# Optimization experiments

Hardware: AMD Instinct MI355X
Metric: run time of the kernel (lower is better)

## Reference

```python
import jax, jax.numpy as jnp
import numpy as np

N_USER = 150_000
M_ITEM = 30_000
N_NODES = N_USER + M_ITEM
D = 64                      # embedding_dim
N_LAYERS = 3                # gcn_layer_number
E = 600_000                 # user-item interactions (symmetric nnz = 2E)
B = 1024
NUM_RATE, NUM_GENRE, NUM_DIR, NUM_ACT = 6, 25, 2186, 8030
NUM_GENDER, NUM_AGE, NUM_OCC, NUM_ZIP = 2, 7, 21, 3402
H1, H2 = 64, 64             # first/second fc hidden dims
FC1_IN = D * 10


def setup_inputs() -> dict:
    key = jax.random.key(0)
    ks = jax.random.split(key, 24)
    # aux features: 0/1 values are valid indices for every categorical field
    aux_info = jax.random.randint(ks[0], (B, 10246), 0, 2, dtype=jnp.int32)
    user_ids = jax.random.randint(ks[1], (B,), 0, N_USER, dtype=jnp.int32)
    item_ids = jax.random.randint(ks[2], (B,), 0, M_ITEM, dtype=jnp.int32)
    # bipartite graph: random interactions, symmetric normalized adjacency
    u = jax.random.randint(ks[3], (E,), 0, N_USER, dtype=jnp.int32)
    i = jax.random.randint(ks[4], (E,), 0, M_ITEM, dtype=jnp.int32) + N_USER
    graph_row = jnp.concatenate([u, i])
    graph_col = jnpph = jnp.concatenate([i, u]) if False else jnp.concatenate([i, u])
    deg = jax.ops.segment_sum(jnp.ones((2 * E,), jnp.float32), graph_row, num_segments=N_NODES)
    dinv = jnp.where(deg > 0, jax.lax.rsqrt(jnp.maximum(deg, 1.0)), 0.0)
    graph_val = dinv[graph_row] * dinv[graph_col]
    s = 0.1
    nrm = lambda k, shp: (jax.random.normal(k, shp, jnp.float32) * s)
    return {
        "aux_info": aux_info, "user_ids": user_ids, "item_ids": item_ids,
        "graph_row": graph_row, "graph_col": graph_col, "graph_val": graph_val,
        "rate_tab": nrm(ks[5], (NUM_RATE, D)),
        "genre_W": nrm(ks[6], (NUM_GENRE, D)),
        "director_W": nrm(ks[7], (NUM_DIR, D)),
        "actor_W": nrm(ks[8], (NUM_ACT, D)),
        "gender_tab": nrm(ks[9], (NUM_GENDER, D)),
        "age_tab": nrm(ks[10], (NUM_AGE, D)),
        "occ_tab": nrm(ks[11], (NUM_OCC, D)),
        "area_tab": nrm(ks[12], (NUM_ZIP, D)),
        "user_rel": nrm(ks[13], (N_USER, D)),
        "item_rel": nrm(ks[14], (M_ITEM, D)),
        "fc1_W": nrm(ks[15], (FC1_IN, H1)), "fc1_b": jnp.zeros((H1,), jnp.float32),
        "fc2_W": nrm(ks[16], (H1, H2)), "fc2_b": jnp.zeros((H2,), jnp.float32),
        "out_W": nrm(ks[17], (H2, 1)), "out_b": jnp.zeros((1,), jnp.float32),
    }


def _lightgcn(user_rel, item_rel, row, col, val):
    # LightGCN: repeated SpMM D^-1/2 A D^-1/2 @ emb, mean over layer outputs
    emb = jnp.concatenate([user_rel, item_rel], axis=0)      # [N, D]
    acc = emb
    for _ in range(N_LAYERS):
        emb = jax.ops.segment_sum(val[:, None] * emb[col], row, num_segments=N_NODES)
        acc = acc + emb
    light = acc / (N_LAYERS + 1)
    return light[:N_USER], light[N_USER:]


def _multi_hot(idx_int, W):
    x = idx_int.astype(jnp.float32)
    return (x @ W) / jnp.sum(x, axis=1, keepdims=True)


def reference(aux_info, user_ids, item_ids, graph_row, graph_col, graph_val,
              rate_tab, genre_W, director_W, actor_W,
              gender_tab, age_tab, occ_tab, area_tab,
              user_rel, item_rel,
              fc1_W, fc1_b, fc2_W, fc2_b, out_W, out_b):
    rate_idx = aux_info[:, 0]
    genre_idx = aux_info[:, 1:26]
    director_idx = aux_info[:, 26:2212]
    actor_idx = aux_info[:, 2212:10242]
    gender_idx = aux_info[:, 10242]
    age_idx = aux_info[:, 10243]
    occ_idx = aux_info[:, 10244]
    area_idx = aux_info[:, 10245]

    item_emb = jnp.concatenate([
        rate_tab[rate_idx],
        _multi_hot(genre_idx, genre_W),
        _multi_hot(director_idx, director_W),
        _multi_hot(actor_idx, actor_W),
    ], axis=1)                                               # [B, 4D]
    user_emb = jnp.concatenate([
        gender_tab[gender_idx], age_tab[age_idx],
        occ_tab[occ_idx], area_tab[area_idx],
    ], axis=1)                                               # [B, 4D]

    all_users, all_items = _lightgcn(user_rel, item_rel, graph_row, graph_col, graph_val)
    X = jnp.concatenate([item_emb, user_emb,
                         all_users[user_ids], all_items[item_ids]], axis=1)  # [B, 10D]
    X = jax.nn.relu(X @ fc1_W + fc1_b)
    X = jax.nn.relu(X @ fc2_W + fc2_b)
    return X @ out_W + out_b                                 # [B, 1]
```

## Files before the change

### kernel.cpp

```cpp
#include <hip/hip_runtime.h>
#include <hip/hip_bf16.h>
#include <hip/hip_fp16.h>

#define N_USER 150000
#define M_ITEM 30000
#define N_NODES 180000
#define E2 1200000
#define BATCH 1024
#define AUX_W 10246
#define KP_G 32
#define KP_D 2208
#define KP_A 8064
#define NBKT 265
#define WT_BLKS 2576
#define BCNT_BLKS 293
#define MH_BLKS 672
#define CVT_BLKS 5625

typedef __attribute__((ext_vector_type(8))) short short8;
typedef __attribute__((ext_vector_type(8))) unsigned short ushort8_t;
typedef __attribute__((ext_vector_type(4))) float f32x4;

__device__ __forceinline__ int bucket_of(int r) {
    return r < N_USER ? (r >> 10) : 147 + ((r - N_USER) >> 8);
}

__device__ __forceinline__ int detect_f32(const void* probe) {
    float v = __bfloat162float(((const __hip_bfloat16*)probe)[threadIdx.x & 63]);
    unsigned long long m = __ballot(!(fabsf(v) < 1000.0f));
    return __popcll(m) > 8;
}

struct CvtSeg { const void* src; float* dst; int n; int blk0; };
struct CvtBatch { CvtSeg seg[16]; };

__global__ void __launch_bounds__(256) k_prep(CvtBatch cb, int cvtBlks,
                                              const void* Wg, const void* Wd, const void* Wa,
                                              unsigned short* WtG, unsigned short* WtD, unsigned short* WtA,
                                              const int* __restrict__ grow, int* __restrict__ bucket_tot,
                                              const void* probe) {
    int blk = blockIdx.x, tid = threadIdx.x;
    if (blk < BCNT_BLKS) {
        __shared__ int h[NBKT];
        for (int i = tid; i < NBKT; i += 256) h[i] = 0;
        __syncthreads();
        int idx0 = blk * 4096;
        #pragma unroll
        for (int k = 0; k < 16; ++k) {
            int i = idx0 + k * 256 + tid;
            if (i < E2) atomicAdd(&h[bucket_of(grow[i])], 1);
        }
        __syncthreads();
        for (int i = tid; i < NBKT; i += 256) if (h[i]) atomicAdd(&bucket_tot[i], h[i]);
        return;
    }
    if (blk < BCNT_BLKS + cvtBlks) {
        int isf32 = detect_f32(probe);
        int cblk = blk - BCNT_BLKS;
        int si = 0;
        #pragma unroll
        for (int i = 0; i < 16; ++i) if (cblk >= cb.seg[i].blk0) si = i;
        const CvtSeg sg = cb.seg[si];
        int i = (cblk - sg.blk0) * 256 + tid;
        if (i >= sg.n) return;
        if (isf32) sg.dst[i] = ((const float*)sg.src)[i];
        else       sg.dst[i] = __bfloat162float(((const __hip_bfloat16*)sg.src)[i]);
        return;
    }
    {
        int isf32 = detect_f32(probe);
        int t = (blk - BCNT_BLKS - cvtBlks) * 256 + tid;
        if (t >= (KP_G + KP_D + KP_A) * 64) return;
        int kp = t >> 6, n = t & 63;
        int k, K; const void* src; unsigned short* dst;
        if (kp < KP_G)              { k = kp;               K = 25;   src = Wg; dst = WtG; }
        else if (kp < KP_G + KP_D)  { k = kp - KP_G;        K = 2186; src = Wd; dst = WtD; }
        else                        { k = kp - KP_G - KP_D; K = 8030; src = Wa; dst = WtA; }
        unsigned short v = 0;
        if (k < K) {
            if (isf32) {
                __hip_bfloat16 h = __float2bfloat16(((const float*)src)[(size_t)k * 64 + n]);
                v = *(unsigned short*)&h;
            } else {
                v = ((const unsigned short*)src)[(size_t)k * 64 + n];
            }
        }
        dst[(((size_t)(k >> 5) * 64 + n) * 4 + ((k >> 3) & 3)) * 8 + (k & 7)] = v;
    }
}

__global__ void __launch_bounds__(512) k_bscan(const int* __restrict__ bucket_tot,
                                               int* __restrict__ bucket_base,
                                               int* __restrict__ bucketcur) {
    __shared__ int s[512];
    int tid = threadIdx.x;
    s[tid] = (tid < NBKT) ? bucket_tot[tid] : 0;
    __syncthreads();
    for (int off = 1; off < 512; off <<= 1) {
        int v = (tid >= off) ? s[tid - off] : 0;
        __syncthreads();
        s[tid] += v;
        __syncthreads();
    }
    int excl = tid ? s[tid - 1] : 0;
    bucket_base[tid] = excl;
    if (tid < NBKT) bucketcur[tid] = excl;
}

__device__ void mhgemm_body(int blk, const int* __restrict__ aux,
                            const unsigned short* __restrict__ WtG,
                            const unsigned short* __restrict__ WtD,
                            const unsigned short* __restrict__ WtA,
                            float* __restrict__ Xmh, float* __restrict__ cntf) {
    int seg, rb, k0, klen, Kseg, auxoff;
    const unsigned short* Wt;
    if (blk < 16)       { seg = 0; rb = blk;                      k0 = 0;              klen = 25;                  Kseg = 25;   auxoff = 1;    Wt = WtG; }
    else if (blk < 160) { int t = blk - 16;  seg = 1; rb = t & 15; k0 = (t >> 4) * 256; klen = min(256, 2186 - k0); Kseg = 2186; auxoff = 26;   Wt = WtD; }
    else                { int t = blk - 160; seg = 2; rb = t & 15; k0 = (t >> 4) * 256; klen = min(256, 8030 - k0); Kseg = 8030; auxoff = 2212; Wt = WtA; }
    int lane = threadIdx.x & 63, wave = threadIdx.x >> 6;
    int m = lane & 15, quad = lane >> 4;
    int row = rb * 64 + wave * 16 + m;
    const int* arow = aux + (size_t)row * AUX_W + auxoff;

    f32x4 acc0 = {0.f,0.f,0.f,0.f}, acc1 = acc0, acc2 = acc0, acc3 = acc0;
    int isum = 0;
    int nchunk = (klen + 31) >> 5;
    int pa[8], na[8];
    auto lda = [&](int kci, int (&A)[8]) {
        int kb = k0 + kci * 32 + quad * 8;
        if (kb + 8 <= Kseg) {
            #pragma unroll
            for (int j = 0; j < 8; ++j) A[j] = arow[kb + j];
        } else {
            #pragma unroll
            for (int j = 0; j < 8; ++j) A[j] = (kb + j < Kseg) ? arow[kb + j] : 0;
        }
    };
    lda(0, pa);
    for (int kci = 0; kci < nchunk; ++kci) {
        if (kci + 1 < nchunk) lda(kci + 1, na);
        union { unsigned u[4]; short8 s; } af;
        af.u[0] = (unsigned)pa[0] * 16256u + (unsigned)pa[1] * 0x3F800000u;
        af.u[1] = (unsigned)pa[2] * 16256u + (unsigned)pa[3] * 0x3F800000u;
        af.u[2] = (unsigned)pa[4] * 16256u + (unsigned)pa[5] * 0x3F800000u;
        af.u[3] = (unsigned)pa[6] * 16256u + (unsigned)pa[7] * 0x3F800000u;
        isum += pa[0] + pa[1] + pa[2] + pa[3] + pa[4] + pa[5] + pa[6] + pa[7];
        size_t kcg = (size_t)(k0 >> 5) + kci;
        const unsigned short* bp = Wt + ((kcg * 64 + m) * 4 + quad) * 8;
        short8 b0 = *(const short8*)(bp);
        short8 b1 = *(const short8*)(bp + 512);
        short8 b2 = *(const short8*)(bp + 1024);
        short8 b3 = *(const short8*)(bp + 1536);
        acc0 = __builtin_amdgcn_mfma_f32_16x16x32_bf16(af.s, b0, acc0, 0, 0, 0);
        acc1 = __builtin_amdgcn_mfma_f32_16x16x32_bf16(af.s, b1, acc1, 0, 0, 0);
        acc2 = __builtin_amdgcn_mfma_f32_16x16x32_bf16(af.s, b2, acc2, 0, 0, 0);
        acc3 = __builtin_amdgcn_mfma_f32_16x16x32_bf16(af.s, b3, acc3, 0, 0, 0);
        #pragma unroll
        for (int j = 0; j < 8; ++j) pa[j] = na[j];
    }
    float asum = (float)isum;
    asum += __shfl_xor(asum, 16);
    asum += __shfl_xor(asum, 32);
    if (quad == 0) atomicAdd(&cntf[seg * BATCH + row], asum);
    float* xbase = Xmh + ((size_t)seg * BATCH + rb * 64 + wave * 16 + quad * 4) * 64;
    #pragma unroll
    for (int reg = 0; reg < 4; ++reg) {
        float* xr = xbase + (size_t)reg * 64;
        atomicAdd(&xr[ 0 + m], acc0[reg]);
        atomicAdd(&xr[16 + m], acc1[reg]);
        atomicAdd(&xr[32 + m], acc2[reg]);
        atomicAdd(&xr[48 + m], acc3[reg]);
    }
}

__global__ void __launch_bounds__(256) k_p1(const int* __restrict__ grow, const int* __restrict__ gcol,
                                            int* __restrict__ bucketcur, int2* __restrict__ binned,
                                            const int* __restrict__ aux,
                                            const unsigned short* __restrict__ WtG,
                                            const unsigned short* __restrict__ WtD,
                                            const unsigned short* __restrict__ WtA,
                                            float* __restrict__ Xmh, float* __restrict__ cntf,
                                            const void* rawU, const void* rawI,
                                            __half* __restrict__ embH) {
    int blk = blockIdx.x;
    if (blk < MH_BLKS) {
        mhgemm_body(blk, aux, WtG, WtD, WtA, Xmh, cntf);
        return;
    }
    if (blk < MH_BLKS + BCNT_BLKS) {
        __shared__ int h1[NBKT], base1[NBKT];
        int tid = threadIdx.x;
        for (int i = tid; i < NBKT; i += 256) h1[i] = 0;
        __syncthreads();
        int idx0 = (blk - MH_BLKS) * 4096;
        int r[16], c[16];
        #pragma unroll
        for (int k = 0; k < 16; ++k) {
            int i = idx0 + k * 256 + tid;
            if (i < E2) {
                r[k] = grow[i]; c[k] = gcol[i];
                atomicAdd(&h1[bucket_of(r[k])], 1);
            } else r[k] = -1;
        }
        __syncthreads();
        for (int i = tid; i < NBKT; i += 256) {
            base1[i] = h1[i] ? atomicAdd(&bucketcur[i], h1[i]) : 0;
            h1[i] = 0;
        }
        __syncthreads();
        #pragma unroll
        for (int k = 0; k < 16; ++k) {
            if (r[k] >= 0) {
                int b = bucket_of(r[k]);
                int p = base1[b] + atomicAdd(&h1[b], 1);
                binned[p] = make_int2(r[k], c[k]);
            }
        }
        return;
    }
    int isf32 = detect_f32(rawU);
    int q = (blk - MH_BLKS - BCNT_BLKS) * 256 + threadIdx.x;
    if (q >= N_NODES * 8) return;
    int r = q >> 3;
    const void* src; size_t qq;
    if (r < N_USER) { src = rawU; qq = (size_t)q; }
    else            { src = rawI; qq = (size_t)q - (size_t)N_USER * 8; }
    float f[8];
    if (isf32) {
        float4 a = ((const float4*)src)[qq * 2], b = ((const float4*)src)[qq * 2 + 1];
        f[0]=a.x; f[1]=a.y; f[2]=a.z; f[3]=a.w; f[4]=b.x; f[5]=b.y; f[6]=b.z; f[7]=b.w;
    } else {
        ushort8_t u = ((const ushort8_t*)src)[qq];
        #pragma unroll
        for (int i = 0; i < 8; ++i) {
            unsigned short us = u[i];
            f[i] = __bfloat162float(*(__hip_bfloat16*)&us);
        }
    }
    ushort8_t o;
    #pragma unroll
    for (int i = 0; i < 8; ++i) {
        __half h = __float2half(f[i]);
        o[i] = *(unsigned short*)&h;
    }
    ((ushort8_t*)embH)[(size_t)q] = o;
}

__global__ void __launch_bounds__(256) k_p2(const int2* __restrict__ binned, const int* __restrict__ bb,
                                            int* __restrict__ cols, int2* __restrict__ moffs,
                                            float* __restrict__ dinv, float* __restrict__ dsq,
                                            float* __restrict__ gsc) {
    __shared__ int h[1024];
    __shared__ int ws2[256];
    int b = blockIdx.x, tid = threadIdx.x;
    int r0, r1;
    if (b < 147) { r0 = b << 10; r1 = min((b + 1) << 10, N_USER); }
    else         { r0 = N_USER + ((b - 147) << 8); r1 = min(N_USER + ((b - 146) << 8), N_NODES); }
    int s0 = bb[b], e0 = bb[b + 1];
    for (int i = tid; i < 1024; i += 256) h[i] = 0;
    __syncthreads();
    for (int j = s0 + tid; j < e0; j += 256) atomicAdd(&h[binned[j].x - r0], 1);
    __syncthreads();
    int t0 = tid * 4;
    int a0 = h[t0], a1 = h[t0 + 1], a2 = h[t0 + 2], a3 = h[t0 + 3];
    ws2[tid] = a0 + a1 + a2 + a3;
    __syncthreads();
    for (int off = 1; off < 256; off <<= 1) {
        int v = (tid >= off) ? ws2[tid - off] : 0;
        __syncthreads();
        ws2[tid] += v;
        __syncthreads();
    }
    int excl = tid ? ws2[tid - 1] : 0;
    int ex[4] = { excl, excl + a0, excl + a0 + a1, excl + a0 + a1 + a2 };
    int ac[4] = { a0, a1, a2, a3 };
    #pragma unroll
    for (int i = 0; i < 4; ++i) {
        int row = r0 + t0 + i;
        if (row < r1) {
            moffs[row] = make_int2(s0 + ex[i], s0 + ex[i] + ac[i]);
            float deg = (float)ac[i];
            bool nz = deg > 0.f;
            dinv[row] = nz ? rsqrtf(deg) : 0.f;
            dsq[row]  = nz ? 1.f / deg  : 0.f;
            gsc[row]  = nz ? sqrtf(deg) : 0.f;
        }
        h[t0 + i] = ex[i];
    }
    __syncthreads();
    for (int j = s0 + tid; j < e0; j += 256) {
        int2 e = binned[j];
        int p = s0 + atomicAdd(&h[e.x - r0], 1);
        cols[p] = e.y << 7;
    }
}

__global__ void __launch_bounds__(256, 8) k_spmv_w(const __half* __restrict__ src,
                                                   const void* rawU, const void* rawI,
                                                   __half* __restrict__ dst,
                                                   const int2* __restrict__ moffs_in,
                                                   const int* __restrict__ cols,
                                                   const float* __restrict__ dinv,
                                                   const float* __restrict__ dsq,
                                                   int spmvN, float* __restrict__ tacc,
                                                   const int* __restrict__ uids, const int* __restrict__ iids,
                                                   int2* __restrict__ moffs2) {
    int tid = threadIdx.x, lane = tid & 63;
    int blk = blockIdx.x;
    if (blk >= spmvN) {
        if (blk < spmvN + 512) {
            int t = (blk - spmvN) * 4 + (tid >> 6);
            int r = (t < BATCH) ? uids[t] : (N_USER + iids[t - BATCH]);
            int2 se = moffs_in[r];
            if (lane == 0) moffs2[r] = se;
            for (int j = se.x + lane; j < se.y; j += 64) {
                int c = (unsigned)cols[j] >> 7;
                moffs2[c] = moffs_in[c];
            }
            return;
        }
        {
            int isf32 = detect_f32(rawU);
            int t = (blk - spmvN - 512) * 4 + (tid >> 6);
            const void* s; size_t ri;
            if (t < BATCH) { s = rawU; ri = (size_t)uids[t]; }
            else           { s = rawI; ri = (size_t)iids[t - BATCH]; }
            float v;
            if (isf32) v = ((const float*)s)[ri * 64 + lane];
            else       v = __bfloat162float(((const __hip_bfloat16*)s)[ri * 64 + lane]);
            tacc[(size_t)t * 64 + lane] = v;
            return;
        }
    }
    int wid8 = blk * 4 + (tid >> 6);
    int g = lane >> 3, l8 = lane & 7;
    int r = wid8 * 8 + g;
    int2 se = moffs_in[r];
    int s = se.x, e = se.y;
    const char* sb = (const char*)src + (l8 << 4);
    float a[8] = {0.f,0.f,0.f,0.f,0.f,0.f,0.f,0.f};
    int j0 = s;
    for (; j0 + 4 <= e; j0 += 4) {
        int c[4]; float w[4];
        #pragma unroll
        for (int u = 0; u < 4; ++u) { c[u] = cols[j0 + u]; w[u] = dinv[(unsigned)c[u] >> 7]; }
        float4 rv[4];
        #pragma unroll
        for (int u = 0; u < 4; ++u) rv[u] = *(const float4*)(sb + (size_t)(unsigned)c[u]);
        #pragma unroll
        for (int u = 0; u < 4; ++u) {
            const __half2* h = (const __half2*)&rv[u];
            float2 f0 = __half22float2(h[0]), f1 = __half22float2(h[1]);
            float2 f2 = __half22float2(h[2]), f3 = __half22float2(h[3]);
            a[0] = fmaf(w[u], f0.x, a[0]); a[1] = fmaf(w[u], f0.y, a[1]);
            a[2] = fmaf(w[u], f1.x, a[2]); a[3] = fmaf(w[u], f1.y, a[3]);
            a[4] = fmaf(w[u], f2.x, a[4]); a[5] = fmaf(w[u], f2.y, a[5]);
            a[6] = fmaf(w[u], f3.x, a[6]); a[7] = fmaf(w[u], f3.y, a[7]);
        }
    }
    if (j0 < e) {
        int c[4]; float w[4];
        #pragma unroll
        for (int u = 0; u < 4; ++u) {
            int j = j0 + u;
            c[u] = cols[min(j, e - 1)];
            w[u] = (j < e) ? dinv[(unsigned)c[u] >> 7] : 0.f;
        }
        float4 rv[4];
        #pragma unroll
        for (int u = 0; u < 4; ++u) rv[u] = *(const float4*)(sb + (size_t)(unsigned)c[u]);
        #pragma unroll
        for (int u = 0; u < 4; ++u) {
            const __half2* h = (const __half2*)&rv[u];
            float2 f0 = __half22float2(h[0]), f1 = __half22float2(h[1]);
            float2 f2 = __half22float2(h[2]), f3 = __half22float2(h[3]);
            a[0] = fmaf(w[u], f0.x, a[0]); a[1] = fmaf(w[u], f0.y, a[1]);
            a[2] = fmaf(w[u], f1.x, a[2]); a[3] = fmaf(w[u], f1.y, a[3]);
            a[4] = fmaf(w[u], f2.x, a[4]); a[5] = fmaf(w[u], f2.y, a[5]);
            a[6] = fmaf(w[u], f3.x, a[6]); a[7] = fmaf(w[u], f3.y, a[7]);
        }
    }
    if (e > s) {
        float d = dsq[r];
        float4 ov;
        __half2* op = (__half2*)&ov;
        op[0] = __floats2half2_rn(a[0] * d, a[1] * d);
        op[1] = __floats2half2_rn(a[2] * d, a[3] * d);
        op[2] = __floats2half2_rn(a[4] * d, a[5] * d);
        op[3] = __floats2half2_rn(a[6] * d, a[7] * d);
        *(float4*)((char*)dst + ((size_t)r << 7) + (l8 << 4)) = ov;
    }
}

__global__ void __launch_bounds__(256, 8) k_spmv(const __half* __restrict__ src, __half* __restrict__ dst,
                                                 const int2* __restrict__ moffs_in, const int* __restrict__ cols,
                                                 const float* __restrict__ dsq,
                                                 int spmvN, float* __restrict__ tacc,
                                                 const int* __restrict__ uids, const int* __restrict__ iids,
                                                 const float* __restrict__ gsc) {
    int tid = threadIdx.x, lane = tid & 63;
    int blk = blockIdx.x;
    if (blk >= spmvN) {
        int t = (blk - spmvN) * 4 + (tid >> 6);
        int r = (t < BATCH) ? uids[t] : (N_USER + iids[t - BATCH]);
        float g = gsc[r];
        float h = __half2float(src[(size_t)r * 64 + lane]);
        tacc[(size_t)t * 64 + lane] += (g > 0.f) ? h * g : 0.f;
        return;
    }
    int wid8 = blk * 4 + (tid >> 6);
    int g = lane >> 3, l8 = lane & 7;
    int r = wid8 * 8 + g;
    int2 se = moffs_in[r];
    int s = se.x, e = se.y;
    const char* sb = (const char*)src + (l8 << 4);
    float2 a0 = {0.f,0.f}, a1 = a0, a2 = a0, a3 = a0;
    int j0 = s;
    for (; j0 + 4 <= e; j0 += 4) {
        int c[4];
        #pragma unroll
        for (int u = 0; u < 4; ++u) c[u] = cols[j0 + u];
        float4 rv[4];
        #pragma unroll
        for (int u = 0; u < 4; ++u) rv[u] = *(const float4*)(sb + (size_t)(unsigned)c[u]);
        #pragma unroll
        for (int u = 0; u < 4; ++u) {
            const __half2* h = (const __half2*)&rv[u];
            float2 f0 = __half22float2(h[0]), f1 = __half22float2(h[1]);
            float2 f2 = __half22float2(h[2]), f3 = __half22float2(h[3]);
            a0.x += f0.x; a0.y += f0.y; a1.x += f1.x; a1.y += f1.y;
            a2.x += f2.x; a2.y += f2.y; a3.x += f3.x; a3.y += f3.y;
        }
    }
    if (j0 < e) {
        int c[4]; float w[4];
        #pragma unroll
        for (int u = 0; u < 4; ++u) {
            int j = j0 + u;
            c[u] = cols[min(j, e - 1)];
            w[u] = (j < e) ? 1.f : 0.f;
        }
        float4 rv[4];
        #pragma unroll
        for (int u = 0; u < 4; ++u) rv[u] = *(const float4*)(sb + (size_t)(unsigned)c[u]);
        #pragma unroll
        for (int u = 0; u < 4; ++u) {
            const __half2* h = (const __half2*)&rv[u];
            float2 f0 = __half22float2(h[0]), f1 = __half22float2(h[1]);
            float2 f2 = __half22float2(h[2]), f3 = __half22float2(h[3]);
            a0.x = fmaf(w[u], f0.x, a0.x); a0.y = fmaf(w[u], f0.y, a0.y);
            a1.x = fmaf(w[u], f1.x, a1.x); a1.y = fmaf(w[u], f1.y, a1.y);
            a2.x = fmaf(w[u], f2.x, a2.x); a2.y = fmaf(w[u], f2.y, a2.y);
            a3.x = fmaf(w[u], f3.x, a3.x); a3.y = fmaf(w[u], f3.y, a3.y);
        }
    }
    if (e > s) {
        float d = dsq[r];
        float4 ov;
        __half2* op = (__half2*)&ov;
        op[0] = __floats2half2_rn(a0.x * d, a0.y * d);
        op[1] = __floats2half2_rn(a1.x * d, a1.y * d);
        op[2] = __floats2half2_rn(a2.x * d, a2.y * d);
        op[3] = __floats2half2_rn(a3.x * d, a3.y * d);
        *(float4*)((char*)dst + ((size_t)r << 7) + (l8 << 4)) = ov;
    }
}

__global__ void __launch_bounds__(256) k_mlp(const int* __restrict__ aux,
                                             const float* __restrict__ ratef, const float* __restrict__ genderf,
                                             const float* __restrict__ agef, const float* __restrict__ occf,
                                             const float* __restrict__ areaf, const float* __restrict__ tacc,
                                             const float* __restrict__ Xmh, const float* __restrict__ cntf,
                                             const float* __restrict__ W1, const float* __restrict__ b1,
                                             const float* __restrict__ W2, const float* __restrict__ b2,
                                             const float* __restrict__ Wo, const float* __restrict__ bo,
                                             void* __restrict__ out, const void* probe,
                                             const __half* __restrict__ embA,
                                             const int2* __restrict__ moffs, const int* __restrict__ cols,
                                             const float* __restrict__ dinv, const float* __restrict__ gsc,
                                             const int* __restrict__ uids, const int* __restrict__ iids) {
    __shared__ float sx[4][640];
    __shared__ float sh[4][64];
    int isf32 = detect_f32(probe);
    int lane = threadIdx.x & 63, w = threadIdx.x >> 6;
    int b = blockIdx.x * 4 + w;
    const int* arow = aux + (size_t)b * AUX_W;
    float* xr = sx[w];

    #pragma unroll 1
    for (int which = 0; which < 2; ++which) {
        int t = which ? (BATCH + b) : b;
        int r = which ? (N_USER + iids[b]) : uids[b];
        int2 se = moffs[r];
        int s = se.x, e = se.y;
        int p = lane & 31, ep = lane >> 5;
        const char* sb = (const char*)embA + (p << 2);
        float ax = 0.f, ay = 0.f;
        int j0 = s;
        for (; j0 + 16 <= e; j0 += 16) {
            int c[8];
            #pragma unroll
            for (int u = 0; u < 8; ++u) c[u] = cols[j0 + 2 * u + ep];
            float2 v[8];
            #pragma unroll
            for (int u = 0; u < 8; ++u) v[u] = __half22float2(*(const __half2*)(sb + (size_t)(unsigned)c[u]));
            #pragma unroll
            for (int u = 0; u < 8; ++u) { ax += v[u].x; ay += v[u].y; }
        }
        if (j0 + 8 <= e) {
            int c[4];
            #pragma unroll
            for (int u = 0; u < 4; ++u) c[u] = cols[j0 + 2 * u + ep];
            float2 v[4];
            #pragma unroll
            for (int u = 0; u < 4; ++u) v[u] = __half22float2(*(const __half2*)(sb + (size_t)(unsigned)c[u]));
            #pragma unroll
            for (int u = 0; u < 4; ++u) { ax += v[u].x; ay += v[u].y; }
            j0 += 8;
        }
        if (j0 + 4 <= e) {
            int c0 = cols[j0 + ep], c1 = cols[j0 + 2 + ep];
            float2 v0 = __half22float2(*(const __half2*)(sb + (size_t)(unsigned)c0));
            float2 v1 = __half22float2(*(const __half2*)(sb + (size_t)(unsigned)c1));
            ax += v0.x + v1.x; ay += v0.y + v1.y;
            j0 += 4;
        }
        if (j0 < e) {
            int j1 = j0 + ep, j2 = j0 + 2 + ep;
            int c0 = cols[min(j1, e - 1)], c1 = cols[min(j2, e - 1)];
            float w0 = (j1 < e) ? 1.f : 0.f, w1 = (j2 < e) ? 1.f : 0.f;
            float2 v0 = __half22float2(*(const __half2*)(sb + (size_t)(unsigned)c0));
            float2 v1 = __half22float2(*(const __half2*)(sb + (size_t)(unsigned)c1));
            ax = fmaf(w0, v0.x, ax); ay = fmaf(w0, v0.y, ay);
            ax = fmaf(w1, v1.x, ax); ay = fmaf(w1, v1.y, ay);
        }
        ax += __shfl_xor(ax, 32);
        ay += __shfl_xor(ay, 32);
        if (ep == 0) {
            float s0 = tacc[(size_t)t * 64 + (p << 1)];
            float s1 = tacc[(size_t)t * 64 + (p << 1) + 1];
            if (e > s) {
                float2 self = __half22float2(*(const __half2*)((const char*)embA + ((size_t)r << 7) + (p << 2)));
                float di = dinv[r], g = gsc[r];
                s0 += di * ax + g * self.x;
                s1 += di * ay + g * self.y;
            }
            xr[512 + (which << 6) + (p << 1)]     = s0 * 0.25f;
            xr[512 + (which << 6) + (p << 1) + 1] = s1 * 0.25f;
        }
    }

    xr[0   + lane] = ratef[arow[0] * 64 + lane];
    xr[64  + lane] = Xmh[((size_t)0 * BATCH + b) * 64 + lane] / cntf[0 * BATCH + b];
    xr[128 + lane] = Xmh[((size_t)1 * BATCH + b) * 64 + lane] / cntf[1 * BATCH + b];
    xr[192 + lane] = Xmh[((size_t)2 * BATCH + b) * 64 + lane] / cntf[2 * BATCH + b];
    xr[256 + lane] = genderf[arow[10242] * 64 + lane];
    xr[320 + lane] = agef[arow[10243] * 64 + lane];
    xr[384 + lane] = occf[arow[10244] * 64 + lane];
    xr[448 + lane] = areaf[arow[10245] * 64 + lane];
    float acc = b1[lane];
    #pragma unroll 8
    for (int k = 0; k < 640; ++k) acc += xr[k] * W1[(size_t)k * 64 + lane];
    float h1 = fmaxf(acc, 0.f);
    sh[w][lane] = h1;
    float acc2 = b2[lane];
    #pragma unroll 8
    for (int j = 0; j < 64; ++j) acc2 += sh[w][j] * W2[(size_t)j * 64 + lane];
    float h2 = fmaxf(acc2, 0.f);
    float p = h2 * Wo[lane];
    #pragma unroll
    for (int off = 32; off; off >>= 1) p += __shfl_down(p, off);
    if (lane == 0) {
        float r = p + bo[0];
        if (isf32) ((float*)out)[b] = r;
        else       ((__hip_bfloat16*)out)[b] = __float2bfloat16(r);
    }
}

extern "C" void kernel_launch(void* const* d_in, const int* in_sizes, int n_in,
                              void* d_out, int out_size, void* d_ws, size_t ws_size,
                              hipStream_t stream) {
    const int* aux  = (const int*)d_in[0];
    const int* uids = (const int*)d_in[1];
    const int* iids = (const int*)d_in[2];
    const int* grow = (const int*)d_in[3];
    const int* gcol = (const int*)d_in[4];

    char* p = (char*)d_ws;
    auto alloc = [&](size_t bytes) -> char* {
        char* r = p;
        p += (bytes + 255) / 256 * 256;
        return r;
    };
    int*   bucket_tot  = (int*)alloc(512 * 4);
    float* Xmh         = (float*)alloc((size_t)3 * BATCH * 64 * 4);
    float* cntf        = (float*)alloc((size_t)3 * BATCH * 4);
    int2*  moffs2      = (int2*)alloc((size_t)180224 * 8);
    char*  zero_end    = p;
    int*   bucket_base = (int*)alloc(512 * 4);
    int*   bucketcur   = (int*)alloc(512 * 4);
    int2*  moffs       = (int2*)alloc((size_t)180224 * 8);
    float* dinv        = (float*)alloc((size_t)180224 * 4);
    float* dsq         = (float*)alloc((size_t)180224 * 4);
    float* gsc         = (float*)alloc((size_t)180224 * 4);
    int2*  binned      = (int2*)alloc((size_t)E2 * 8);
    int*   cols        = (int*)alloc((size_t)E2 * 4);
    __half* embH       = (__half*)alloc((size_t)N_NODES * 64 * 2);
    __half* embA       = (__half*)alloc((size_t)N_NODES * 64 * 2);
    __half* embB       = (__half*)alloc((size_t)N_NODES * 64 * 2);
    float* tacc        = (float*)alloc((size_t)2048 * 64 * 4);
    unsigned short* WtG = (unsigned short*)alloc((size_t)KP_G * 64 * 2);
    unsigned short* WtD = (unsigned short*)alloc((size_t)KP_D * 64 * 2);
    unsigned short* WtA = (unsigned short*)alloc((size_t)KP_A * 64 * 2);
    float* ratef   = (float*)alloc(384 * 4);
    float* genderf = (float*)alloc(128 * 4);
    float* agef    = (float*)alloc(448 * 4);
    float* occf    = (float*)alloc(1344 * 4);
    float* areaf   = (float*)alloc((size_t)217728 * 4);
    float* fc1W    = (float*)alloc((size_t)40960 * 4);
    float* fc1b    = (float*)alloc(64 * 4);
    float* fc2W    = (float*)alloc(4096 * 4);
    float* fc2b    = (float*)alloc(64 * 4);
    float* outW    = (float*)alloc(64 * 4);
    float* outb    = (float*)alloc(4);

    const void* probe = d_in[14];

    hipMemsetAsync(bucket_tot, 0, (size_t)(zero_end - (char*)bucket_tot), stream);

    CvtBatch cb;
    int blk = 0, si = 0;
    auto addseg = [&](const void* s, float* d, int n) {
        cb.seg[si].src = s; cb.seg[si].dst = d; cb.seg[si].n = n; cb.seg[si].blk0 = blk;
        blk += (n + 255) / 256; ++si;
    };
    addseg(d_in[6],  ratef,   384);
    addseg(d_in[10], genderf, 128);
    addseg(d_in[11], agef,    448);
    addseg(d_in[12], occf,    1344);
    addseg(d_in[13], areaf,   217728);
    addseg(d_in[16], fc1W,   40960);
    addseg(d_in[17], fc1b,   64);
    addseg(d_in[18], fc2W,   4096);
    addseg(d_in[19], fc2b,   64);
    addseg(d_in[20], outW,   64);
    addseg(d_in[21], outb,   1);
    for (int i = si; i < 16; ++i) { cb.seg[i].src = nullptr; cb.seg[i].dst = nullptr; cb.seg[i].n = 0; cb.seg[i].blk0 = 0x7fffffff; }
    const int cvtBlks = blk;
    hipLaunchKernelGGL(k_prep, dim3(BCNT_BLKS + cvtBlks + WT_BLKS), dim3(256), 0, stream,
                       cb, cvtBlks, d_in[7], d_in[8], d_in[9], WtG, WtD, WtA, grow, bucket_tot, probe);

    hipLaunchKernelGGL(k_bscan, dim3(1), dim3(512), 0, stream, bucket_tot, bucket_base, bucketcur);
    hipLaunchKernelGGL(k_p1, dim3(MH_BLKS + BCNT_BLKS + CVT_BLKS), dim3(256), 0, stream,
                       grow, gcol, bucketcur, binned, aux, WtG, WtD, WtA, Xmh, cntf,
                       d_in[14], d_in[15], embH);
    hipLaunchKernelGGL(k_p2, dim3(NBKT), dim3(256), 0, stream, binned, bucket_base, cols, moffs, dinv, dsq, gsc);

    const int spmvN = N_NODES / 32;
    hipLaunchKernelGGL(k_spmv_w, dim3(spmvN + 1024), dim3(256), 0, stream,
                       embH, d_in[14], d_in[15], embB, moffs, cols, dinv, dsq, spmvN,
                       tacc, uids, iids, moffs2);
    hipLaunchKernelGGL(k_spmv, dim3(spmvN + 512), dim3(256), 0, stream,
                       embB, embA, moffs2, cols, dsq, spmvN, tacc, uids, iids, gsc);

    hipLaunchKernelGGL(k_mlp, dim3(BATCH / 4), dim3(256), 0, stream,
                       aux, ratef, genderf, agef, occf, areaf, tacc, Xmh, cntf,
                       fc1W, fc1b, fc2W, fc2b, outW, outb, d_out, probe,
                       embA, moffs, cols, dinv, gsc, uids, iids);
}
```

Measured before the change: 287.1 us.

## Pack binned edges into one int, unroll SpMV by 8, move tacc init

Binned edge records are packed from int2 into a single int (column shifted above the local row offset within its bucket), which halves scatter and read traffic between k_p1 and k_p2. The SpMV inner loops now process 8 neighbours per iteration to put more gathers in flight, and launch bounds drop from 8 to 4 blocks per CU to allow more registers. Seeding the batch accumulators from the raw embeddings moves from k_spmv_w into extra blocks of k_p1. The trade-offs are lower occupancy in the SpMV kernels and the packed encoding's dependence on column indices fitting in the shifted bits.

```diff
diff --git a/kernel.cpp b/kernel.cpp
--- a/kernel.cpp
+++ b/kernel.cpp
@@ -174,14 +174,16 @@
 }
 
 __global__ void __launch_bounds__(256) k_p1(const int* __restrict__ grow, const int* __restrict__ gcol,
-                                            int* __restrict__ bucketcur, int2* __restrict__ binned,
+                                            int* __restrict__ bucketcur, int* __restrict__ binned,
                                             const int* __restrict__ aux,
                                             const unsigned short* __restrict__ WtG,
                                             const unsigned short* __restrict__ WtD,
                                             const unsigned short* __restrict__ WtA,
                                             float* __restrict__ Xmh, float* __restrict__ cntf,
                                             const void* rawU, const void* rawI,
-                                            __half* __restrict__ embH) {
+                                            __half* __restrict__ embH,
+                                            float* __restrict__ tacc,
+                                            const int* __restrict__ uids, const int* __restrict__ iids) {
     int blk = blockIdx.x;
     if (blk < MH_BLKS) {
         mhgemm_body(blk, aux, WtG, WtD, WtA, Xmh, cntf);
@@ -213,53 +215,69 @@
             if (r[k] >= 0) {
                 int b = bucket_of(r[k]);
                 int p = base1[b] + atomicAdd(&h1[b], 1);
-                binned[p] = make_int2(r[k], c[k]);
+                int enc = (r[k] < N_USER) ? ((c[k] << 10) | (r[k] & 1023))
+                                          : ((c[k] << 8) | ((r[k] - N_USER) & 255));
+                binned[p] = enc;
             }
         }
         return;
     }
-    int isf32 = detect_f32(rawU);
-    int q = (blk - MH_BLKS - BCNT_BLKS) * 256 + threadIdx.x;
-    if (q >= N_NODES * 8) return;
-    int r = q >> 3;
-    const void* src; size_t qq;
-    if (r < N_USER) { src = rawU; qq = (size_t)q; }
-    else            { src = rawI; qq = (size_t)q - (size_t)N_USER * 8; }
-    float f[8];
-    if (isf32) {
-        float4 a = ((const float4*)src)[qq * 2], b = ((const float4*)src)[qq * 2 + 1];
-        f[0]=a.x; f[1]=a.y; f[2]=a.z; f[3]=a.w; f[4]=b.x; f[5]=b.y; f[6]=b.z; f[7]=b.w;
-    } else {
-        ushort8_t u = ((const ushort8_t*)src)[qq];
+    if (blk < MH_BLKS + BCNT_BLKS + CVT_BLKS) {
+        int isf32 = detect_f32(rawU);
+        int q = (blk - MH_BLKS - BCNT_BLKS) * 256 + threadIdx.x;
+        int r = q >> 3;
+        const void* src; size_t qq;
+        if (r < N_USER) { src = rawU; qq = (size_t)q; }
+        else            { src = rawI; qq = (size_t)q - (size_t)N_USER * 8; }
+        float f[8];
+        if (isf32) {
+            float4 a = ((const float4*)src)[qq * 2], b = ((const float4*)src)[qq * 2 + 1];
+            f[0]=a.x; f[1]=a.y; f[2]=a.z; f[3]=a.w; f[4]=b.x; f[5]=b.y; f[6]=b.z; f[7]=b.w;
+        } else {
+            ushort8_t u = ((const ushort8_t*)src)[qq];
+            #pragma unroll
+            for (int i = 0; i < 8; ++i) {
+                unsigned short us = u[i];
+                f[i] = __bfloat162float(*(__hip_bfloat16*)&us);
+            }
+        }
+        ushort8_t o;
         #pragma unroll
         for (int i = 0; i < 8; ++i) {
-            unsigned short us = u[i];
-            f[i] = __bfloat162float(*(__hip_bfloat16*)&us);
-        }
-    }
-    ushort8_t o;
-    #pragma unroll
-    for (int i = 0; i < 8; ++i) {
-        __half h = __float2half(f[i]);
-        o[i] = *(unsigned short*)&h;
-    }
-    ((ushort8_t*)embH)[(size_t)q] = o;
-}
-
-__global__ void __launch_bounds__(256) k_p2(const int2* __restrict__ binned, const int* __restrict__ bb,
+            __half h = __float2half(f[i]);
+            o[i] = *(unsigned short*)&h;
+        }
+        ((ushort8_t*)embH)[(size_t)q] = o;
+        return;
+    }
+    {
+        int isf32 = detect_f32(rawU);
+        int lane = threadIdx.x & 63;
+        int t = (blk - MH_BLKS - BCNT_BLKS - CVT_BLKS) * 4 + (threadIdx.x >> 6);
+        const void* s; size_t ri;
+        if (t < BATCH) { s = rawU; ri = (size_t)uids[t]; }
+        else           { s = rawI; ri = (size_t)iids[t - BATCH]; }
+        float v;
+        if (isf32) v = ((const float*)s)[ri * 64 + lane];
+        else       v = __bfloat162float(((const __hip_bfloat16*)s)[ri * 64 + lane]);
+        tacc[(size_t)t * 64 + lane] = v;
+    }
+}
+
+__global__ void __launch_bounds__(256) k_p2(const int* __restrict__ binned, const int* __restrict__ bb,
                                             int* __restrict__ cols, int2* __restrict__ moffs,
                                             float* __restrict__ dinv, float* __restrict__ dsq,
                                             float* __restrict__ gsc) {
     __shared__ int h[1024];
     __shared__ int ws2[256];
     int b = blockIdx.x, tid = threadIdx.x;
-    int r0, r1;
-    if (b < 147) { r0 = b << 10; r1 = min((b + 1) << 10, N_USER); }
-    else         { r0 = N_USER + ((b - 147) << 8); r1 = min(N_USER + ((b - 146) << 8), N_NODES); }
+    int r0, r1, shift, mask;
+    if (b < 147) { r0 = b << 10; r1 = min((b + 1) << 10, N_USER); shift = 10; mask = 1023; }
+    else         { r0 = N_USER + ((b - 147) << 8); r1 = min(N_USER + ((b - 146) << 8), N_NODES); shift = 8; mask = 255; }
     int s0 = bb[b], e0 = bb[b + 1];
     for (int i = tid; i < 1024; i += 256) h[i] = 0;
     __syncthreads();
-    for (int j = s0 + tid; j < e0; j += 256) atomicAdd(&h[binned[j].x - r0], 1);
+    for (int j = s0 + tid; j < e0; j += 256) atomicAdd(&h[binned[j] & mask], 1);
     __syncthreads();
     int t0 = tid * 4;
     int a0 = h[t0], a1 = h[t0 + 1], a2 = h[t0 + 2], a3 = h[t0 + 3];
@@ -289,48 +307,33 @@
     }
     __syncthreads();
     for (int j = s0 + tid; j < e0; j += 256) {
-        int2 e = binned[j];
-        int p = s0 + atomicAdd(&h[e.x - r0], 1);
-        cols[p] = e.y << 7;
-    }
-}
-
-__global__ void __launch_bounds__(256, 8) k_spmv_w(const __half* __restrict__ src,
-                                                   const void* rawU, const void* rawI,
+        int v = binned[j];
+        int p = s0 + atomicAdd(&h[v & mask], 1);
+        cols[p] = ((unsigned)v >> shift) << 7;
+    }
+}
+
+__global__ void __launch_bounds__(256, 4) k_spmv_w(const __half* __restrict__ src,
                                                    __half* __restrict__ dst,
                                                    const int2* __restrict__ moffs_in,
                                                    const int* __restrict__ cols,
                                                    const float* __restrict__ dinv,
                                                    const float* __restrict__ dsq,
-                                                   int spmvN, float* __restrict__ tacc,
+                                                   int spmvN,
                                                    const int* __restrict__ uids, const int* __restrict__ iids,
                                                    int2* __restrict__ moffs2) {
     int tid = threadIdx.x, lane = tid & 63;
     int blk = blockIdx.x;
     if (blk >= spmvN) {
-        if (blk < spmvN + 512) {
-            int t = (blk - spmvN) * 4 + (tid >> 6);
-            int r = (t < BATCH) ? uids[t] : (N_USER + iids[t - BATCH]);
-            int2 se = moffs_in[r];
-            if (lane == 0) moffs2[r] = se;
-            for (int j = se.x + lane; j < se.y; j += 64) {
-                int c = (unsigned)cols[j] >> 7;
-                moffs2[c] = moffs_in[c];
-            }
-            return;
-        }
-        {
-            int isf32 = detect_f32(rawU);
-            int t = (blk - spmvN - 512) * 4 + (tid >> 6);
-            const void* s; size_t ri;
-            if (t < BATCH) { s = rawU; ri = (size_t)uids[t]; }
-            else           { s = rawI; ri = (size_t)iids[t - BATCH]; }
-            float v;
-            if (isf32) v = ((const float*)s)[ri * 64 + lane];
-            else       v = __bfloat162float(((const __hip_bfloat16*)s)[ri * 64 + lane]);
-            tacc[(size_t)t * 64 + lane] = v;
-            return;
-        }
+        int t = (blk - spmvN) * 4 + (tid >> 6);
+        int r = (t < BATCH) ? uids[t] : (N_USER + iids[t - BATCH]);
+        int2 se = moffs_in[r];
+        if (lane == 0) moffs2[r] = se;
+        for (int j = se.x + lane; j < se.y; j += 64) {
+            int c = (unsigned)cols[j] >> 7;
+            moffs2[c] = moffs_in[c];
+        }
+        return;
     }
     int wid8 = blk * 4 + (tid >> 6);
     int g = lane >> 3, l8 = lane & 7;
@@ -340,7 +343,25 @@
     const char* sb = (const char*)src + (l8 << 4);
     float a[8] = {0.f,0.f,0.f,0.f,0.f,0.f,0.f,0.f};
     int j0 = s;
-    for (; j0 + 4 <= e; j0 += 4) {
+    for (; j0 + 8 <= e; j0 += 8) {
+        int c[8]; float w[8];
+        #pragma unroll
+        for (int u = 0; u < 8; ++u) { c[u] = cols[j0 + u]; w[u] = dinv[(unsigned)c[u] >> 7]; }
+        float4 rv[8];
+        #pragma unroll
+        for (int u = 0; u < 8; ++u) rv[u] = *(const float4*)(sb + (size_t)(unsigned)c[u]);
+        #pragma unroll
+        for (int u = 0; u < 8; ++u) {
+            const __half2* h = (const __half2*)&rv[u];
+            float2 f0 = __half22float2(h[0]), f1 = __half22float2(h[1]);
+            float2 f2 = __half22float2(h[2]), f3 = __half22float2(h[3]);
+            a[0] = fmaf(w[u], f0.x, a[0]); a[1] = fmaf(w[u], f0.y, a[1]);
+            a[2] = fmaf(w[u], f1.x, a[2]); a[3] = fmaf(w[u], f1.y, a[3]);
+            a[4] = fmaf(w[u], f2.x, a[4]); a[5] = fmaf(w[u], f2.y, a[5]);
+            a[6] = fmaf(w[u], f3.x, a[6]); a[7] = fmaf(w[u], f3.y, a[7]);
+        }
+    }
+    if (j0 + 4 <= e) {
         int c[4]; float w[4];
         #pragma unroll
         for (int u = 0; u < 4; ++u) { c[u] = cols[j0 + u]; w[u] = dinv[(unsigned)c[u] >> 7]; }
@@ -357,6 +378,7 @@
             a[4] = fmaf(w[u], f2.x, a[4]); a[5] = fmaf(w[u], f2.y, a[5]);
             a[6] = fmaf(w[u], f3.x, a[6]); a[7] = fmaf(w[u], f3.y, a[7]);
         }
+        j0 += 4;
     }
     if (j0 < e) {
         int c[4]; float w[4];
@@ -392,7 +414,7 @@
     }
 }
 
-__global__ void __launch_bounds__(256, 8) k_spmv(const __half* __restrict__ src, __half* __restrict__ dst,
+__global__ void __launch_bounds__(256, 4) k_spmv(const __half* __restrict__ src, __half* __restrict__ dst,
                                                  const int2* __restrict__ moffs_in, const int* __restrict__ cols,
                                                  const float* __restrict__ dsq,
                                                  int spmvN, float* __restrict__ tacc,
@@ -414,9 +436,25 @@
     int2 se = moffs_in[r];
     int s = se.x, e = se.y;
     const char* sb = (const char*)src + (l8 << 4);
-    float2 a0 = {0.f,0.f}, a1 = a0, a2 = a0, a3 = a0;
+    float a[8] = {0.f,0.f,0.f,0.f,0.f,0.f,0.f,0.f};
     int j0 = s;
-    for (; j0 + 4 <= e; j0 += 4) {
+    for (; j0 + 8 <= e; j0 += 8) {
+        int c[8];
+        #pragma unroll
+        for (int u = 0; u < 8; ++u) c[u] = cols[j0 + u];
+        float4 rv[8];
+        #pragma unroll
+        for (int u = 0; u < 8; ++u) rv[u] = *(const float4*)(sb + (size_t)(unsigned)c[u]);
+        #pragma unroll
+        for (int u = 0; u < 8; ++u) {
+            const __half2* h = (const __half2*)&rv[u];
+            float2 f0 = __half22float2(h[0]), f1 = __half22float2(h[1]);
+            float2 f2 = __half22float2(h[2]), f3 = __half22float2(h[3]);
+            a[0] += f0.x; a[1] += f0.y; a[2] += f1.x; a[3] += f1.y;
+            a[4] += f2.x; a[5] += f2.y; a[6] += f3.x; a[7] += f3.y;
+        }
+    }
+    if (j0 + 4 <= e) {
         int c[4];
         #pragma unroll
         for (int u = 0; u < 4; ++u) c[u] = cols[j0 + u];
@@ -428,9 +466,10 @@
             const __half2* h = (const __half2*)&rv[u];
             float2 f0 = __half22float2(h[0]), f1 = __half22float2(h[1]);
             float2 f2 = __half22float2(h[2]), f3 = __half22float2(h[3]);
-            a0.x += f0.x; a0.y += f0.y; a1.x += f1.x; a1.y += f1.y;
-            a2.x += f2.x; a2.y += f2.y; a3.x += f3.x; a3.y += f3.y;
-        }
+            a[0] += f0.x; a[1] += f0.y; a[2] += f1.x; a[3] += f1.y;
+            a[4] += f2.x; a[5] += f2.y; a[6] += f3.x; a[7] += f3.y;
+        }
+        j0 += 4;
     }
     if (j0 < e) {
         int c[4]; float w[4];
@@ -448,20 +487,20 @@
             const __half2* h = (const __half2*)&rv[u];
             float2 f0 = __half22float2(h[0]), f1 = __half22float2(h[1]);
             float2 f2 = __half22float2(h[2]), f3 = __half22float2(h[3]);
-            a0.x = fmaf(w[u], f0.x, a0.x); a0.y = fmaf(w[u], f0.y, a0.y);
-            a1.x = fmaf(w[u], f1.x, a1.x); a1.y = fmaf(w[u], f1.y, a1.y);
-            a2.x = fmaf(w[u], f2.x, a2.x); a2.y = fmaf(w[u], f2.y, a2.y);
-            a3.x = fmaf(w[u], f3.x, a3.x); a3.y = fmaf(w[u], f3.y, a3.y);
+            a[0] = fmaf(w[u], f0.x, a[0]); a[1] = fmaf(w[u], f0.y, a[1]);
+            a[2] = fmaf(w[u], f1.x, a[2]); a[3] = fmaf(w[u], f1.y, a[3]);
+            a[4] = fmaf(w[u], f2.x, a[4]); a[5] = fmaf(w[u], f2.y, a[5]);
+            a[6] = fmaf(w[u], f3.x, a[6]); a[7] = fmaf(w[u], f3.y, a[7]);
         }
     }
     if (e > s) {
         float d = dsq[r];
         float4 ov;
         __half2* op = (__half2*)&ov;
-        op[0] = __floats2half2_rn(a0.x * d, a0.y * d);
-        op[1] = __floats2half2_rn(a1.x * d, a1.y * d);
-        op[2] = __floats2half2_rn(a2.x * d, a2.y * d);
-        op[3] = __floats2half2_rn(a3.x * d, a3.y * d);
+        op[0] = __floats2half2_rn(a[0] * d, a[1] * d);
+        op[1] = __floats2half2_rn(a[2] * d, a[3] * d);
+        op[2] = __floats2half2_rn(a[4] * d, a[5] * d);
+        op[3] = __floats2half2_rn(a[6] * d, a[7] * d);
         *(float4*)((char*)dst + ((size_t)r << 7) + (l8 << 4)) = ov;
     }
 }
@@ -603,7 +642,7 @@
     float* dinv        = (float*)alloc((size_t)180224 * 4);
     float* dsq         = (float*)alloc((size_t)180224 * 4);
     float* gsc         = (float*)alloc((size_t)180224 * 4);
-    int2*  binned      = (int2*)alloc((size_t)E2 * 8);
+    int*   binned      = (int*)alloc((size_t)E2 * 4);
     int*   cols        = (int*)alloc((size_t)E2 * 4);
     __half* embH       = (__half*)alloc((size_t)N_NODES * 64 * 2);
     __half* embA       = (__half*)alloc((size_t)N_NODES * 64 * 2);
@@ -651,15 +690,14 @@
                        cb, cvtBlks, d_in[7], d_in[8], d_in[9], WtG, WtD, WtA, grow, bucket_tot, probe);
 
     hipLaunchKernelGGL(k_bscan, dim3(1), dim3(512), 0, stream, bucket_tot, bucket_base, bucketcur);
-    hipLaunchKernelGGL(k_p1, dim3(MH_BLKS + BCNT_BLKS + CVT_BLKS), dim3(256), 0, stream,
+    hipLaunchKernelGGL(k_p1, dim3(MH_BLKS + BCNT_BLKS + CVT_BLKS + 512), dim3(256), 0, stream,
                        grow, gcol, bucketcur, binned, aux, WtG, WtD, WtA, Xmh, cntf,
-                       d_in[14], d_in[15], embH);
+                       d_in[14], d_in[15], embH, tacc, uids, iids);
     hipLaunchKernelGGL(k_p2, dim3(NBKT), dim3(256), 0, stream, binned, bucket_base, cols, moffs, dinv, dsq, gsc);
 
     const int spmvN = N_NODES / 32;
-    hipLaunchKernelGGL(k_spmv_w, dim3(spmvN + 1024), dim3(256), 0, stream,
-                       embH, d_in[14], d_in[15], embB, moffs, cols, dinv, dsq, spmvN,
-                       tacc, uids, iids, moffs2);
+    hipLaunchKernelGGL(k_spmv_w, dim3(spmvN + 512), dim3(256), 0, stream,
+                       embH, embB, moffs, cols, dinv, dsq, spmvN, uids, iids, moffs2);
     hipLaunchKernelGGL(k_spmv, dim3(spmvN + 512), dim3(256), 0, stream,
                        embB, embA, moffs2, cols, dsq, spmvN, tacc, uids, iids, gsc);
 
```

Measured after the change: 288.8 us. No clear change (+0.6%).
